# Kernel optimization log

Hardware: AMD Instinct MI355X
Metric: run time of the kernel (lower is better)

The kernel has to match this reference:

```python
import jax, jax.numpy as jnp
import numpy as np

N_NODES = 100000
N_EDGES = 1600000
IN_F, HID, OUT = 256, 32, 16


def setup_inputs() -> dict:
    key = jax.random.key(0)
    ks = jax.random.split(key, 10)
    x = jax.random.normal(ks[0], (N_NODES, IN_F), dtype=jnp.float32)
    edge_index = jax.random.randint(ks[1], (2, N_EDGES), 0, N_NODES, dtype=jnp.int32)
    s = lambda fan_in: 1.0 / np.sqrt(fan_in)
    # Linear params stored torch-style: weight [out, in], bias [out]
    w1a_w = jax.random.uniform(ks[2], (HID, IN_F), jnp.float32, -s(IN_F), s(IN_F))
    w1a_b = jax.random.uniform(ks[3], (HID,), jnp.float32, -s(IN_F), s(IN_F))
    w1b_w = jax.random.uniform(ks[4], (HID, HID), jnp.float32, -s(HID), s(HID))
    w1b_b = jax.random.uniform(ks[5], (HID,), jnp.float32, -s(HID), s(HID))
    w2a_w = jax.random.uniform(ks[6], (OUT, HID), jnp.float32, -s(HID), s(HID))
    w2a_b = jax.random.uniform(ks[7], (OUT,), jnp.float32, -s(HID), s(HID))
    w2b_w = jax.random.uniform(ks[8], (OUT, OUT), jnp.float32, -s(OUT), s(OUT))
    w2b_b = jax.random.uniform(ks[9], (OUT,), jnp.float32, -s(OUT), s(OUT))
    return {"x": x, "w1a_w": w1a_w, "w1a_b": w1a_b, "w1b_w": w1b_w, "w1b_b": w1b_b,
            "w2a_w": w2a_w, "w2a_b": w2a_b, "w2b_w": w2b_w, "w2b_b": w2b_b,
            "edge_index": edge_index}


def _simple_layer(x, wa_w, wa_b, wb_w, wb_b, src, dst):
    h = x @ wa_w.T + wa_b                         # [N, out_ch]
    f_new = h @ wb_w.T + wb_b                     # [N, out_ch]
    agg = jax.ops.segment_sum(h[src], dst, num_segments=x.shape[0])
    return f_new + agg


def reference(x, w1a_w, w1a_b, w1b_w, w1b_b, w2a_w, w2a_b, w2b_w, w2b_b, edge_index):
    src, dst = edge_index[0], edge_index[1]
    h = _simple_layer(x, w1a_w, w1a_b, w1b_w, w1b_b, src, dst)
    h = jax.nn.relu(h)
    # dropout is identity in eval mode (training=False)
    h = _simple_layer(h, w2a_w, w2a_b, w2b_w, w2b_b, src, dst)
    return jax.nn.log_softmax(h, axis=1)
```

## Files before the change

### kernel.cpp

```cpp
#include <hip/hip_runtime.h>
#include <hip/hip_bf16.h>
#include <math.h>

#define N_NODES 100000
#define N_EDGES 1600000
#define IN_F 256
#define HID 32
#define OUTC 16
#define NBUCK 1000
#define BUCK_W 100
#define NBB 256
#define CHUNK 6250
#define MAXE 4096
#define K1_BLOCKS ((N_NODES + 63) / 64)

typedef unsigned short ushort_t;
typedef unsigned int uint_t;
typedef __attribute__((ext_vector_type(8))) short bf16x8;
typedef __attribute__((ext_vector_type(4))) float f32x4;

__device__ inline ushort_t f2bf(float f) {
    union { float f; uint_t u; } v; v.f = f;
    uint_t r = v.u + 0x7fff + ((v.u >> 16) & 1);
    return (ushort_t)(r >> 16);
}
__device__ inline float bf2f(ushort_t h) {
    union { uint_t u; float f; } v; v.u = (uint_t)h << 16;
    return v.f;
}
__device__ inline float bf_lo(uint_t d) {
    union { uint_t u; float f; } v; v.u = d << 16;
    return v.f;
}
__device__ inline float bf_hi(uint_t d) {
    union { uint_t u; float f; } v; v.u = d & 0xFFFF0000u;
    return v.f;
}
__device__ inline bf16x8 packA(const float4& lo, const float4& hi) {
    bf16x8 a;
    a[0] = (short)f2bf(lo.x); a[1] = (short)f2bf(lo.y);
    a[2] = (short)f2bf(lo.z); a[3] = (short)f2bf(lo.w);
    a[4] = (short)f2bf(hi.x); a[5] = (short)f2bf(hi.y);
    a[6] = (short)f2bf(hi.z); a[7] = (short)f2bf(hi.w);
    return a;
}

__global__ __launch_bounds__(256) void k_cnt_wfuse(
    const int* __restrict__ ei, int* __restrict__ bhist,
    const float* __restrict__ w1a_w, const float* __restrict__ w1a_b,
    const float* __restrict__ w1b_w, const float* __restrict__ w1b_b,
    ushort_t* __restrict__ wpack, float* __restrict__ bp)
{
    __shared__ char smem[32 * 1024 + 4 * 1024 + 256];
    const int t = threadIdx.x;

    if (blockIdx.x < NBB) {
        int* lh = (int*)smem;
        const int blk = blockIdx.x;
        for (int b = t; b < NBUCK; b += 256) lh[b] = 0;
        __syncthreads();
        const int base = blk * CHUNK;
        for (int i = t; i < CHUNK; i += 256) {
            const int dst = ei[N_EDGES + base + i];
            atomicAdd(&lh[dst / BUCK_W], 1);
        }
        __syncthreads();
        for (int b = t; b < NBUCK; b += 256) bhist[b * NBB + blk] = lh[b];
        return;
    }

    float (*wps)[256] = (float (*)[256])smem;
    float (*wb_s)[32] = (float (*)[32])(smem + 32 * 1024);
    float* ba_s       = (float*)(smem + 36 * 1024);
    for (int i = t; i < 1024; i += 256) wb_s[i >> 5][i & 31] = w1b_w[i];
    if (t < 32) ba_s[t] = w1a_b[t];
    __syncthreads();
    const int k = t;
    for (int o = 0; o < 32; ++o) {
        float s = 0.f;
        #pragma unroll 8
        for (int c = 0; c < 32; ++c) s += wb_s[o][c] * w1a_w[c * 256 + k];
        wps[o][k] = s;
    }
    if (t < 32) {
        float s = 0.f;
        for (int c = 0; c < 32; ++c) s += wb_s[t][c] * ba_s[c];
        bp[t] = s + w1b_b[t];
    }
    __syncthreads();
    for (int idx = t; idx < 4 * 8 * 64 * 8; idx += 256) {
        const int j  = idx & 7;
        const int l  = (idx >> 3) & 63;
        const int ks = (idx >> 9) & 7;
        const int q  = idx >> 12;
        const int ncol = ((q & 1) << 4) + (l & 15);
        const int krow = ks * 32 + ((l >> 4) << 3) + j;
        const float v = (q < 2) ? w1a_w[ncol * 256 + krow] : wps[ncol][krow];
        wpack[idx] = f2bf(v);
    }
}

__global__ __launch_bounds__(256) void k_scanH(const int* __restrict__ bhist,
                                               int* __restrict__ boffB, int* __restrict__ btot)
{
    __shared__ int sh[256];
    const int t = threadIdx.x;
    const int b = blockIdx.x;
    const int v = bhist[b * NBB + t];
    sh[t] = v;
    __syncthreads();
    #pragma unroll
    for (int off = 1; off < 256; off <<= 1) {
        const int u = (t >= off) ? sh[t - off] : 0;
        __syncthreads();
        sh[t] += u;
        __syncthreads();
    }
    boffB[b * NBB + t] = sh[t] - v;
    if (t == 255) btot[b] = sh[255];
}

__global__ __launch_bounds__(1024) void k_scanH2(const int* __restrict__ btot,
                                                 int* __restrict__ bstart)
{
    __shared__ int sh[1024];
    const int t = threadIdx.x;
    const int v = (t < NBUCK) ? btot[t] : 0;
    sh[t] = v;
    __syncthreads();
    #pragma unroll
    for (int off = 1; off < 1024; off <<= 1) {
        const int u = (t >= off) ? sh[t - off] : 0;
        __syncthreads();
        sh[t] += u;
        __syncthreads();
    }
    if (t < NBUCK) bstart[t] = sh[t] - v;
    if (t == NBUCK - 1) bstart[NBUCK] = sh[t];
}

__global__ __launch_bounds__(256) void k_scat_k1(
    const int* __restrict__ ei,
    const int* __restrict__ boffB, const int* __restrict__ bstart,
    int* __restrict__ pairsP,
    const float* __restrict__ x,
    const float* __restrict__ w1a_b, const float* __restrict__ bp,
    const ushort_t* __restrict__ wpack,
    ushort_t* __restrict__ h1b, float* __restrict__ out1)
{
    __shared__ char arena[32 * 1024];
    const int t = threadIdx.x;

    if (blockIdx.x < NBB) {
        int* lcur = (int*)arena;
        const int blk = blockIdx.x;
        for (int b = t; b < NBUCK; b += 256) lcur[b] = bstart[b] + boffB[b * NBB + blk];
        __syncthreads();
        const int base = blk * CHUNK;
        for (int i = t; i < CHUNK; i += 256) {
            const int src = ei[base + i];
            const int dst = ei[N_EDGES + base + i];
            const int b = dst / BUCK_W;
            const int pos = atomicAdd(&lcur[b], 1);
            pairsP[pos] = ((dst - b * BUCK_W) << 17) | src;
        }
        return;
    }

    bf16x8* wl = (bf16x8*)arena;
    {
        const uint4* src = (const uint4*)wpack;
        uint4* dst = (uint4*)arena;
        #pragma unroll
        for (int i = 0; i < 8; ++i) dst[t + i * 256] = src[t + i * 256];
    }
    __syncthreads();

    const int lane = t & 63;
    const int wv = t >> 6;
    const int node0 = (int)(blockIdx.x - NBB) * 64 + wv * 16;

    const int arow = lane & 15;
    const int kq   = lane >> 4;
    int nodeA = node0 + arow;
    if (nodeA >= N_NODES) nodeA = N_NODES - 1;

    const float* xr = x + (size_t)nodeA * IN_F + kq * 8;

    f32x4 accA0 = {0.f, 0.f, 0.f, 0.f};
    f32x4 accA1 = {0.f, 0.f, 0.f, 0.f};
    f32x4 accB0 = {0.f, 0.f, 0.f, 0.f};
    f32x4 accB1 = {0.f, 0.f, 0.f, 0.f};

    #pragma unroll
    for (int ks = 0; ks < 8; ++ks) {
        const float4 xlo = *(const float4*)(xr + ks * 32);
        const float4 xhi = *(const float4*)(xr + ks * 32 + 4);
        const bf16x8 a = packA(xlo, xhi);
        const bf16x8 bA0 = wl[(0 * 8 + ks) * 64 + lane];
        const bf16x8 bA1 = wl[(1 * 8 + ks) * 64 + lane];
        const bf16x8 bB0 = wl[(2 * 8 + ks) * 64 + lane];
        const bf16x8 bB1 = wl[(3 * 8 + ks) * 64 + lane];
        accA0 = __builtin_amdgcn_mfma_f32_16x16x32_bf16(a, bA0, accA0, 0, 0, 0);
        accA1 = __builtin_amdgcn_mfma_f32_16x16x32_bf16(a, bA1, accA1, 0, 0, 0);
        accB0 = __builtin_amdgcn_mfma_f32_16x16x32_bf16(a, bB0, accB0, 0, 0, 0);
        accB1 = __builtin_amdgcn_mfma_f32_16x16x32_bf16(a, bB1, accB1, 0, 0, 0);
    }

    const int ch = lane & 15;
    const int rbase = (lane >> 4) * 4;
    const float ba0 = w1a_b[ch];
    const float ba1 = w1a_b[ch + 16];
    const float bb0 = bp[ch];
    const float bb1 = bp[ch + 16];

    #pragma unroll
    for (int r = 0; r < 4; ++r) {
        const int node = node0 + rbase + r;
        if (node < N_NODES) {
            h1b[(size_t)node * HID + ch]       = f2bf(accA0[r] + ba0);
            h1b[(size_t)node * HID + ch + 16]  = f2bf(accA1[r] + ba1);
            out1[(size_t)node * HID + ch]      = accB0[r] + bb0;
            out1[(size_t)node * HID + ch + 16] = accB1[r] + bb1;
        }
    }
}

__global__ __launch_bounds__(512) void k_agg32(const int* __restrict__ bstart,
                                               const int* __restrict__ pairsP,
                                               const ushort_t* __restrict__ h1b,
                                               float* __restrict__ out1,
                                               int* __restrict__ colg,
                                               int* __restrict__ offg)
{
    __shared__ int cnt[128];
    __shared__ int off[129];
    __shared__ int srt[MAXE];
    const int t = threadIdx.x;
    const int b = blockIdx.x;
    const int c2 = t & 15;
    const int grp = t >> 4;
    const uint_t* h1u = (const uint_t*)h1b;

    const int e0g = bstart[b];
    const int e1g = bstart[b + 1];
    const bool single = (e1g - e0g) <= MAXE;

    for (int ch0 = e0g; ch0 < e1g; ch0 += MAXE) {
        const int ce = (ch0 + MAXE < e1g) ? (ch0 + MAXE) : e1g;
        const int cn = ce - ch0;

        if (t < 128) cnt[t] = 0;
        __syncthreads();
        for (int i = t; i < cn; i += 512)
            atomicAdd(&cnt[pairsP[ch0 + i] >> 17], 1);
        __syncthreads();
        {
            int v = (t < 128) ? cnt[t] : 0;
            if (t < 128) off[t] = v;
            __syncthreads();
            #pragma unroll
            for (int o = 1; o < 128; o <<= 1) {
                int u = 0;
                if (t < 128 && t >= o) u = off[t - o];
                __syncthreads();
                if (t < 128) off[t] += u;
                __syncthreads();
            }
            if (t < 128) {
                const int inc = off[t];
                off[t] = inc - v;
                cnt[t] = inc - v;
                if (t == 127) off[128] = inc;
            }
        }
        __syncthreads();
        for (int i = t; i < cn; i += 512) {
            const int p = pairsP[ch0 + i];
            const int pos = atomicAdd(&cnt[p >> 17], 1);
            srt[pos] = p & 0x1FFFF;
        }
        __syncthreads();
        if (single) {
            for (int i = t; i < cn; i += 512) colg[ch0 + i] = srt[i];
            if (t <= BUCK_W) offg[b * (BUCK_W + 1) + t] = e0g + off[t];
        }
        for (int n = grp; n < BUCK_W; n += 32) {
            const int e0 = off[n];
            const int e1 = off[n + 1];
            float l0 = 0.f, h0 = 0.f, l1 = 0.f, h1 = 0.f;
            int e = e0;
            for (; e + 4 <= e1; e += 4) {
                const uint_t u0 = h1u[(size_t)srt[e]     * 16 + c2];
                const uint_t u1 = h1u[(size_t)srt[e + 1] * 16 + c2];
                const uint_t u2 = h1u[(size_t)srt[e + 2] * 16 + c2];
                const uint_t u3 = h1u[(size_t)srt[e + 3] * 16 + c2];
                l0 += bf_lo(u0); h0 += bf_hi(u0);
                l1 += bf_lo(u1); h1 += bf_hi(u1);
                l0 += bf_lo(u2); h0 += bf_hi(u2);
                l1 += bf_lo(u3); h1 += bf_hi(u3);
            }
            for (; e < e1; ++e) {
                const uint_t u = h1u[(size_t)srt[e] * 16 + c2];
                l0 += bf_lo(u); h0 += bf_hi(u);
            }
            float2* o = (float2*)&out1[((size_t)b * BUCK_W + n) * HID + 2 * c2];
            const float2 cur = *o;
            float2 nv;
            nv.x = fmaxf(cur.x + l0 + l1, 0.f);
            nv.y = fmaxf(cur.y + h0 + h1, 0.f);
            *o = nv;
        }
        __syncthreads();
    }
}

__global__ __launch_bounds__(256) void k3_layer2_dense(
    const float* __restrict__ out1,
    const float* __restrict__ w2a_w, const float* __restrict__ w2a_b,
    const float* __restrict__ w2b_w, const float* __restrict__ w2b_b,
    ushort_t* __restrict__ h2b, float* __restrict__ out2)
{
    __shared__ float rs[64][33];
    __shared__ float h2s[64][17];
    __shared__ float wa[16][33];
    __shared__ float wb[16][17];

    const int t = threadIdx.x;
    const int node0 = blockIdx.x * 64;
    const int nrem = N_NODES - node0;

    for (int i = t; i < 16 * 32; i += 256)
        wa[i >> 5][i & 31] = w2a_w[i];
    if (t < 16 * 16) wb[t >> 4][t & 15] = w2b_w[t];
    for (int i = t; i < 64 * 32; i += 256) {
        int r = i >> 5, c = i & 31;
        float v = 0.f;
        if (r < nrem) v = out1[(size_t)(node0 + r) * HID + c];
        rs[r][c] = fmaxf(v, 0.f);
    }
    __syncthreads();

    const int o = t & 15;
    const int g = t >> 4;

    const float ba = w2a_b[o];
    float acc[4] = {};
    for (int c = 0; c < 32; ++c) {
        const float w = wa[o][c];
        #pragma unroll
        for (int j = 0; j < 4; ++j) acc[j] += rs[g * 4 + j][c] * w;
    }
    #pragma unroll
    for (int j = 0; j < 4; ++j) {
        const int ln = g * 4 + j;
        const float v = acc[j] + ba;
        h2s[ln][o] = v;
        if (ln < nrem) h2b[(size_t)(node0 + ln) * OUTC + o] = f2bf(v);
    }
    __syncthreads();

    const float bbv = w2b_b[o];
    float f[4] = {};
    for (int c = 0; c < 16; ++c) {
        const float w = wb[o][c];
        #pragma unroll
        for (int j = 0; j < 4; ++j) f[j] += h2s[g * 4 + j][c] * w;
    }
    #pragma unroll
    for (int j = 0; j < 4; ++j) {
        const int ln = g * 4 + j;
        if (ln < nrem) out2[(size_t)(node0 + ln) * OUTC + o] = f[j] + bbv;
    }
}

__global__ __launch_bounds__(512) void k_agg16_sm(const int* __restrict__ bstart,
                                                  const int* __restrict__ pairsP,
                                                  const int* __restrict__ colg,
                                                  const int* __restrict__ offg,
                                                  const ushort_t* __restrict__ h2b,
                                                  float* __restrict__ out2)
{
    const int t = threadIdx.x;
    const int b = blockIdx.x;
    const int e0g = bstart[b];
    const int e1g = bstart[b + 1];
    const uint_t* h2u = (const uint_t*)h2b;

    if (e1g - e0g <= MAXE) {
        const int c2 = t & 7;
        const int grp = t >> 3;
        const int ob = b * (BUCK_W + 1);
        for (int n = grp; n < BUCK_W; n += 64) {
            const int e0 = offg[ob + n];
            const int e1 = offg[ob + n + 1];
            float l0 = 0.f, h0 = 0.f, l1 = 0.f, h1v = 0.f;
            int e = e0;
            for (; e + 4 <= e1; e += 4) {
                const uint_t u0 = h2u[(size_t)colg[e]     * 8 + c2];
                const uint_t u1 = h2u[(size_t)colg[e + 1] * 8 + c2];
                const uint_t u2 = h2u[(size_t)colg[e + 2] * 8 + c2];
                const uint_t u3 = h2u[(size_t)colg[e + 3] * 8 + c2];
                l0 += bf_lo(u0); h0 += bf_hi(u0);
                l1 += bf_lo(u1); h1v += bf_hi(u1);
                l0 += bf_lo(u2); h0 += bf_hi(u2);
                l1 += bf_lo(u3); h1v += bf_hi(u3);
            }
            for (; e < e1; ++e) {
                const uint_t u = h2u[(size_t)colg[e] * 8 + c2];
                l0 += bf_lo(u); h0 += bf_hi(u);
            }

            float2* op = (float2*)&out2[((size_t)b * BUCK_W + n) * OUTC + 2 * c2];
            const float2 cur = *op;
            const float v0 = cur.x + l0 + l1;
            const float v1 = cur.y + h0 + h1v;

            float m = fmaxf(v0, v1);
            #pragma unroll
            for (int o = 4; o > 0; o >>= 1)
                m = fmaxf(m, __shfl_xor(m, o, 8));
            float s = expf(v0 - m) + expf(v1 - m);
            #pragma unroll
            for (int o = 4; o > 0; o >>= 1)
                s += __shfl_xor(s, o, 8);
            const float lse = m + logf(s);
            float2 nv; nv.x = v0 - lse; nv.y = v1 - lse;
            *op = nv;
        }
        return;
    }

    __shared__ int cnt[128];
    __shared__ int off[129];
    __shared__ int srt[MAXE];
    const int c = t & 15;
    const int grp = t >> 4;

    for (int ch0 = e0g; ch0 < e1g; ch0 += MAXE) {
        const int ce = (ch0 + MAXE < e1g) ? (ch0 + MAXE) : e1g;
        const int cn = ce - ch0;
        const bool last = (ce == e1g);

        if (t < 128) cnt[t] = 0;
        __syncthreads();
        for (int i = t; i < cn; i += 512)
            atomicAdd(&cnt[pairsP[ch0 + i] >> 17], 1);
        __syncthreads();
        {
            int v = (t < 128) ? cnt[t] : 0;
            if (t < 128) off[t] = v;
            __syncthreads();
            #pragma unroll
            for (int o = 1; o < 128; o <<= 1) {
                int u = 0;
                if (t < 128 && t >= o) u = off[t - o];
                __syncthreads();
                if (t < 128) off[t] += u;
                __syncthreads();
            }
            if (t < 128) {
                const int inc = off[t];
                off[t] = inc - v;
                cnt[t] = inc - v;
                if (t == 127) off[128] = inc;
            }
        }
        __syncthreads();
        for (int i = t; i < cn; i += 512) {
            const int p = pairsP[ch0 + i];
            const int pos = atomicAdd(&cnt[p >> 17], 1);
            srt[pos] = p & 0x1FFFF;
        }
        __syncthreads();

        for (int n = grp; n < BUCK_W; n += 32) {
            const int e0 = off[n];
            const int e1 = off[n + 1];
            float acc = 0.f, acc2 = 0.f;
            int e = e0;
            for (; e + 1 < e1; e += 2) {
                acc += bf2f(h2b[(size_t)srt[e] * OUTC + c]);
                acc2 += bf2f(h2b[(size_t)srt[e + 1] * OUTC + c]);
            }
            if (e < e1) acc += bf2f(h2b[(size_t)srt[e] * OUTC + c]);
            acc += acc2;

            const size_t oidx = ((size_t)b * BUCK_W + n) * OUTC + c;
            if (!last) {
                out2[oidx] += acc;
            } else {
                const float val = out2[oidx] + acc;
                float m = val;
                #pragma unroll
                for (int o = 8; o > 0; o >>= 1)
                    m = fmaxf(m, __shfl_xor(m, o, 16));
                float s = expf(val - m);
                #pragma unroll
                for (int o = 8; o > 0; o >>= 1)
                    s += __shfl_xor(s, o, 16);
                const float lse = m + logf(s);
                out2[oidx] = val - lse;
            }
        }
        __syncthreads();
    }
}

extern "C" void kernel_launch(void* const* d_in, const int* in_sizes, int n_in,
                              void* d_out, int out_size, void* d_ws, size_t ws_size,
                              hipStream_t stream)
{
    const float* x      = (const float*)d_in[0];
    const float* w1a_w  = (const float*)d_in[1];
    const float* w1a_b  = (const float*)d_in[2];
    const float* w1b_w  = (const float*)d_in[3];
    const float* w1b_b  = (const float*)d_in[4];
    const float* w2a_w  = (const float*)d_in[5];
    const float* w2a_b  = (const float*)d_in[6];
    const float* w2b_w  = (const float*)d_in[7];
    const float* w2b_b  = (const float*)d_in[8];
    const int*   ei     = (const int*)d_in[9];
    float* out = (float*)d_out;

    float*    out1   = (float*)d_ws;
    ushort_t* h1b    = (ushort_t*)(out1 + (size_t)N_NODES * HID);
    ushort_t* h2b    = h1b + (size_t)N_NODES * HID;
    int*      pairsP = (int*)(h2b + (size_t)N_NODES * OUTC);
    ushort_t* wpack  = (ushort_t*)(pairsP + N_EDGES);
    float*    bp     = (float*)(wpack + 4 * 8 * 64 * 8);
    int*      bhist  = (int*)(bp + 32);
    int*      boffB  = bhist + NBUCK * NBB;
    int*      btot   = boffB + NBUCK * NBB;
    int*      bstart = btot + NBUCK;
    int*      colg   = bstart + NBUCK + 1;
    int*      offg   = colg + N_EDGES;

    k_cnt_wfuse<<<NBB + 1, 256, 0, stream>>>(ei, bhist,
                                             w1a_w, w1a_b, w1b_w, w1b_b, wpack, bp);
    k_scanH <<<NBUCK, 256, 0, stream>>>(bhist, boffB, btot);
    k_scanH2<<<1, 1024, 0, stream>>>(btot, bstart);
    k_scat_k1<<<NBB + K1_BLOCKS, 256, 0, stream>>>(ei, boffB, bstart, pairsP,
                                                   x, w1a_b, bp, wpack, h1b, out1);
    k_agg32<<<NBUCK, 512, 0, stream>>>(bstart, pairsP, h1b, out1, colg, offg);
    k3_layer2_dense<<<(N_NODES + 63) / 64, 256, 0, stream>>>(out1, w2a_w, w2a_b, w2b_w, w2b_b, h2b, out);
    k_agg16_sm<<<NBUCK, 512, 0, stream>>>(bstart, pairsP, colg, offg, h2b, out);
}
```

Before: 136.9 us.

## Fuse layer-2 dense transform into the 32-channel aggregation kernel

Merges the layer-1 aggregation with the layer-2 dense projections. Each bucket block now loads its 100 nodes' out1 rows into shared memory, accumulates the neighbour sums there, applies ReLU, and computes h2 and out2 in place. This removes one kernel launch and the write-back and re-read of out1 through global memory. In exchange, shared memory use per block grows, so MAXE is lowered to 3072 to compensate, which may send more buckets down the multi-chunk path and reduce occupancy.

```diff
diff --git a/kernel.cpp b/kernel.cpp
--- a/kernel.cpp
+++ b/kernel.cpp
@@ -11,7 +11,7 @@
 #define BUCK_W 100
 #define NBB 256
 #define CHUNK 6250
-#define MAXE 4096
+#define MAXE 3072
 #define K1_BLOCKS ((N_NODES + 63) / 64)
 
 typedef unsigned short ushort_t;
@@ -226,21 +226,34 @@
     }
 }
 
-__global__ __launch_bounds__(512) void k_agg32(const int* __restrict__ bstart,
-                                               const int* __restrict__ pairsP,
-                                               const ushort_t* __restrict__ h1b,
-                                               float* __restrict__ out1,
-                                               int* __restrict__ colg,
-                                               int* __restrict__ offg)
-{
-    __shared__ int cnt[128];
-    __shared__ int off[129];
-    __shared__ int srt[MAXE];
+__global__ __launch_bounds__(512) void k_agg32_l2(
+    const int* __restrict__ bstart, const int* __restrict__ pairsP,
+    const ushort_t* __restrict__ h1b, const float* __restrict__ out1,
+    const float* __restrict__ w2a_w, const float* __restrict__ w2a_b,
+    const float* __restrict__ w2b_w, const float* __restrict__ w2b_b,
+    ushort_t* __restrict__ h2b, float* __restrict__ out2,
+    int* __restrict__ colg, int* __restrict__ offg)
+{
+    __shared__ int   cnt[128];
+    __shared__ int   off[129];
+    __shared__ int   srt[MAXE];
+    __shared__ float rsf[BUCK_W * 33];
+    __shared__ float h2s[BUCK_W * 17];
+    __shared__ float wa[16][33];
+    __shared__ float wb[16][17];
+
     const int t = threadIdx.x;
     const int b = blockIdx.x;
     const int c2 = t & 15;
     const int grp = t >> 4;
+    const int nbase = b * BUCK_W;
     const uint_t* h1u = (const uint_t*)h1b;
+
+    if (t < 512) wa[t >> 5][t & 31] = w2a_w[t];
+    if (t < 256) wb[t >> 4][t & 15] = w2b_w[t];
+    for (int i = t; i < BUCK_W * HID; i += 512)
+        rsf[(i >> 5) * 33 + (i & 31)] = out1[(size_t)nbase * HID + i];
+    __syncthreads();
 
     const int e0g = bstart[b];
     const int e1g = bstart[b + 1];
@@ -304,73 +317,45 @@
                 const uint_t u = h1u[(size_t)srt[e] * 16 + c2];
                 l0 += bf_lo(u); h0 += bf_hi(u);
             }
-            float2* o = (float2*)&out1[((size_t)b * BUCK_W + n) * HID + 2 * c2];
-            const float2 cur = *o;
-            float2 nv;
-            nv.x = fmaxf(cur.x + l0 + l1, 0.f);
-            nv.y = fmaxf(cur.y + h0 + h1, 0.f);
-            *o = nv;
-        }
-        __syncthreads();
-    }
-}
-
-__global__ __launch_bounds__(256) void k3_layer2_dense(
-    const float* __restrict__ out1,
-    const float* __restrict__ w2a_w, const float* __restrict__ w2a_b,
-    const float* __restrict__ w2b_w, const float* __restrict__ w2b_b,
-    ushort_t* __restrict__ h2b, float* __restrict__ out2)
-{
-    __shared__ float rs[64][33];
-    __shared__ float h2s[64][17];
-    __shared__ float wa[16][33];
-    __shared__ float wb[16][17];
-
-    const int t = threadIdx.x;
-    const int node0 = blockIdx.x * 64;
-    const int nrem = N_NODES - node0;
-
-    for (int i = t; i < 16 * 32; i += 256)
-        wa[i >> 5][i & 31] = w2a_w[i];
-    if (t < 16 * 16) wb[t >> 4][t & 15] = w2b_w[t];
-    for (int i = t; i < 64 * 32; i += 256) {
-        int r = i >> 5, c = i & 31;
-        float v = 0.f;
-        if (r < nrem) v = out1[(size_t)(node0 + r) * HID + c];
-        rs[r][c] = fmaxf(v, 0.f);
-    }
-    __syncthreads();
-
-    const int o = t & 15;
-    const int g = t >> 4;
-
-    const float ba = w2a_b[o];
-    float acc[4] = {};
-    for (int c = 0; c < 32; ++c) {
-        const float w = wa[o][c];
-        #pragma unroll
-        for (int j = 0; j < 4; ++j) acc[j] += rs[g * 4 + j][c] * w;
-    }
-    #pragma unroll
-    for (int j = 0; j < 4; ++j) {
-        const int ln = g * 4 + j;
-        const float v = acc[j] + ba;
-        h2s[ln][o] = v;
-        if (ln < nrem) h2b[(size_t)(node0 + ln) * OUTC + o] = f2bf(v);
-    }
-    __syncthreads();
-
-    const float bbv = w2b_b[o];
-    float f[4] = {};
-    for (int c = 0; c < 16; ++c) {
-        const float w = wb[o][c];
-        #pragma unroll
-        for (int j = 0; j < 4; ++j) f[j] += h2s[g * 4 + j][c] * w;
-    }
-    #pragma unroll
-    for (int j = 0; j < 4; ++j) {
-        const int ln = g * 4 + j;
-        if (ln < nrem) out2[(size_t)(node0 + ln) * OUTC + o] = f[j] + bbv;
+            rsf[n * 33 + 2 * c2]     += l0 + l1;
+            rsf[n * 33 + 2 * c2 + 1] += h0 + h1;
+        }
+        __syncthreads();
+    }
+
+    for (int i = t; i < BUCK_W * HID; i += 512) {
+        const int idx = (i >> 5) * 33 + (i & 31);
+        rsf[idx] = fmaxf(rsf[idx], 0.f);
+    }
+    __syncthreads();
+
+    {
+        const int o = t & 15;
+        const int ng = t >> 4;
+        const float ba = w2a_b[o];
+        for (int n = ng; n < BUCK_W; n += 32) {
+            float acc = 0.f;
+            #pragma unroll 8
+            for (int cc = 0; cc < 32; ++cc)
+                acc += rsf[n * 33 + cc] * wa[o][cc];
+            const float v = acc + ba;
+            h2s[n * 17 + o] = v;
+            h2b[(size_t)(nbase + n) * OUTC + o] = f2bf(v);
+        }
+    }
+    __syncthreads();
+
+    {
+        const int o = t & 15;
+        const int ng = t >> 4;
+        const float bbv = w2b_b[o];
+        for (int n = ng; n < BUCK_W; n += 32) {
+            float f = 0.f;
+            #pragma unroll 8
+            for (int cc = 0; cc < 16; ++cc)
+                f += h2s[n * 17 + cc] * wb[o][cc];
+            out2[(size_t)(nbase + n) * OUTC + o] = f + bbv;
+        }
     }
 }
 
@@ -542,7 +527,8 @@
     k_scanH2<<<1, 1024, 0, stream>>>(btot, bstart);
     k_scat_k1<<<NBB + K1_BLOCKS, 256, 0, stream>>>(ei, boffB, bstart, pairsP,
                                                    x, w1a_b, bp, wpack, h1b, out1);
-    k_agg32<<<NBUCK, 512, 0, stream>>>(bstart, pairsP, h1b, out1, colg, offg);
-    k3_layer2_dense<<<(N_NODES + 63) / 64, 256, 0, stream>>>(out1, w2a_w, w2a_b, w2b_w, w2b_b, h2b, out);
+    k_agg32_l2<<<NBUCK, 512, 0, stream>>>(bstart, pairsP, h1b, out1,
+                                          w2a_w, w2a_b, w2b_w, w2b_b,
+                                          h2b, out, colg, offg);
     k_agg16_sm<<<NBUCK, 512, 0, stream>>>(bstart, pairsP, colg, offg, h2b, out);
 }
```

New measurement: 126.4 us (median of 2 runs). 7.7% less time.
